# Kernel optimization log

Hardware: AMD Instinct MI355X
Metric: run time of the kernel (lower is better)

Reference implementation:

```python
import jax, jax.numpy as jnp
import numpy as np

N = 100000
E = 1600000
D_IN = 128
D_HID = 128
D_OUT = 64


def mish(x):
    return x * jnp.tanh(jax.nn.softplus(x))


def sage_conv(x, src, dst, W_l, b_l, W_r):
    # gather source-node features along edges, mean-aggregate at destination
    msg = x[src]  # [E, d]
    agg = jax.ops.segment_sum(msg, dst, num_segments=N)  # [N, d]
    cnt = jax.ops.segment_sum(jnp.ones((E,), x.dtype), dst, num_segments=N)
    agg = agg / jnp.maximum(cnt, 1.0)[:, None]
    # PyG SAGEConv: lin_l(aggregated) + lin_r(root); lin_r has no bias
    return agg @ W_l.T + b_l + x @ W_r.T


def setup_inputs() -> dict:
    key = jax.random.key(0)
    ks = jax.random.split(key, 10)
    s = lambda d: 1.0 / np.sqrt(d)
    return {
        "x": jax.random.normal(ks[0], (N, D_IN), jnp.float32),
        "edge_index": jax.random.randint(ks[1], (2, E), 0, N, jnp.int64),
        "W_l0": jax.random.normal(ks[2], (D_HID, D_IN), jnp.float32) * s(D_IN),
        "b_l0": jnp.zeros((D_HID,), jnp.float32),
        "W_r0": jax.random.normal(ks[3], (D_HID, D_IN), jnp.float32) * s(D_IN),
        "W_l1": jax.random.normal(ks[4], (D_HID, D_HID), jnp.float32) * s(D_HID),
        "b_l1": jnp.zeros((D_HID,), jnp.float32),
        "W_r1": jax.random.normal(ks[5], (D_HID, D_HID), jnp.float32) * s(D_HID),
        "W_head": jax.random.normal(ks[6], (D_OUT, D_HID), jnp.float32) * s(D_HID),
        "b_head": jnp.zeros((D_OUT,), jnp.float32),
    }


def reference(x, edge_index, W_l0, b_l0, W_r0, W_l1, b_l1, W_r1, W_head, b_head):
    src, dst = edge_index[0], edge_index[1]
    h = mish(sage_conv(x, src, dst, W_l0, b_l0, W_r0))  # dropout is identity in eval
    h = mish(sage_conv(h, src, dst, W_l1, b_l1, W_r1))
    return h @ W_head.T + b_head
```

## Files before the change

### kernel.cpp

```cpp
#include <hip/hip_runtime.h>
#include <math.h>

#define N_NODES 100000
#define N_EDGES 1600000
#define DF      128
#define D_HEAD  64

#define NWIN    256
#define WIN_SZ  391
#define NSEG    8
#define CAP_SEG 1024
#define BCH     8192
#define NBUCK   ((N_EDGES + BCH - 1) / BCH)

typedef __attribute__((ext_vector_type(8))) short bf16x8;
typedef __attribute__((ext_vector_type(4))) float f32x4;

static __device__ __forceinline__ float mish_f(float v) {
    float e = __expf(v);
    float q = 1.0f + e;
    float p = q * q;
    float m = v * (p - 1.0f) / (p + 1.0f);
    return (v > 40.0f) ? v : m;
}

static __device__ __forceinline__ unsigned short f2bf(float f) {
    unsigned int u = __builtin_bit_cast(unsigned int, f);
    unsigned int r = (u + 0x7fffu + ((u >> 16) & 1u)) >> 16;
    return (unsigned short)r;
}


__global__ void zero_cnt_kernel(int* __restrict__ bucket_cnt) {
    bucket_cnt[blockIdx.x * 256 + threadIdx.x] = 0;
}


#define XB 12500
#define WB 288

__global__ __launch_bounds__(256) void cvt_bucket_kernel(
        const float* __restrict__ x,
        const float* __restrict__ Wl0, const float* __restrict__ Wr0,
        const float* __restrict__ Wl1, const float* __restrict__ Wr1,
        const float* __restrict__ Wh,
        const int* __restrict__ src, const int* __restrict__ dst,
        unsigned short* __restrict__ xb, unsigned short* __restrict__ wb,
        int* __restrict__ bucket_cnt, unsigned int* __restrict__ pairs) {
    __shared__ int cnt[NWIN][4];
    __shared__ int cur[NWIN][4];
    int b   = blockIdx.x;
    int tid = threadIdx.x;

    if (b >= NBUCK) {
        int cb = b - NBUCK;
        if (cb < XB) {
            int i = cb * 256 + tid;
            float4 v = ((const float4*)x)[i];
            ushort4 o;
            o.x = f2bf(v.x); o.y = f2bf(v.y); o.z = f2bf(v.z); o.w = f2bf(v.w);
            ((ushort4*)xb)[i] = o;
        } else {
            int id = (cb - XB) * 256 + tid;
            if (id < 65536) {
                int seg = id >> 14;
                int r   = id & 16383;
                const float* W = (seg == 0) ? Wl0 : (seg == 1) ? Wr0 : (seg == 2) ? Wl1 : Wr1;
                wb[id] = f2bf(W[r]);
            } else {
                wb[id] = f2bf(Wh[id - 65536]);
            }
        }
        return;
    }

    int set = tid & 3;
    int sg  = b & 7;
    int e0  = b * BCH;
    for (int i = tid; i < NWIN * 4; i += 256) ((int*)cnt)[i] = 0;
    __syncthreads();

    int dc[BCH / 256];
    #pragma unroll 4
    for (int i = 0; i < BCH / 256; ++i) {
        int e = e0 + tid + i * 256;
        int d = (e < N_EDGES) ? dst[e] : -1;
        dc[i] = d;
        if (d >= 0) atomicAdd(&cnt[d / WIN_SZ][set], 1);
    }
    __syncthreads();
    for (int w = tid; w < NWIN; w += 256) {
        int c0 = cnt[w][0], c1 = cnt[w][1], c2 = cnt[w][2], c3 = cnt[w][3];
        int base = atomicAdd(&bucket_cnt[sg * NWIN + w], c0 + c1 + c2 + c3);
        cur[w][0] = base;
        cur[w][1] = base + c0;
        cur[w][2] = base + c0 + c1;
        cur[w][3] = base + c0 + c1 + c2;
    }
    __syncthreads();
    #pragma unroll 4
    for (int i = 0; i < BCH / 256; ++i) {
        int d = dc[i];
        if (d >= 0) {
            int e  = e0 + tid + i * 256;
            int s  = src[e];
            int w  = d / WIN_SZ;
            int dl = d - w * WIN_SZ;
            int idx = atomicAdd(&cur[w][set], 1);
            if (idx < CAP_SEG)
                pairs[((size_t)sg * NWIN + w) * CAP_SEG + idx] = (unsigned)s | ((unsigned)dl << 17);
        }
    }
}


__global__ __launch_bounds__(256) void build_win(const unsigned int* __restrict__ pairs,
                                                 const int* __restrict__ bucket_cnt,
                                                 int* __restrict__ rowstart,
                                                 int* __restrict__ csr) {
    __shared__ int ldeg[WIN_SZ];
    __shared__ int lcsr[NSEG * CAP_SEG];
    __shared__ int tot[NWIN];
    __shared__ int wsum[4];
    __shared__ int red[4];

    int tid = threadIdx.x;
    int w   = blockIdx.x;
    int base_node = w * WIN_SZ;
    int nn = N_NODES - base_node;
    if (nn > WIN_SZ) nn = WIN_SZ;
    if (nn < 0) nn = 0;

    {
        int t = 0;
        #pragma unroll
        for (int s2 = 0; s2 < NSEG; ++s2) {
            int c = bucket_cnt[s2 * NWIN + tid];
            t += (c > CAP_SEG) ? CAP_SEG : c;
        }
        tot[tid] = t;
    }
    for (int i = tid; i < WIN_SZ; i += 256) ldeg[i] = 0;
    __syncthreads();

    int val = (tid < w) ? tot[tid] : 0;
    #pragma unroll
    for (int o = 32; o; o >>= 1) val += __shfl_xor(val, o);
    if ((tid & 63) == 0) red[tid >> 6] = val;
    int ntot = tot[w];
    __syncthreads();
    int ebase = red[0] + red[1] + red[2] + red[3];

    #pragma unroll
    for (int s2 = 0; s2 < NSEG; ++s2) {
        int c = bucket_cnt[s2 * NWIN + w];
        if (c > CAP_SEG) c = CAP_SEG;
        const unsigned int* pw = pairs + ((size_t)s2 * NWIN + w) * CAP_SEG;
        for (int i = tid; i < c; i += 256)
            atomicAdd(&ldeg[pw[i] >> 17], 1);
    }
    __syncthreads();

    int i0 = tid * 2;
    int v[2];
    int s = 0;
    #pragma unroll
    for (int q = 0; q < 2; ++q) {
        v[q] = (i0 + q < nn) ? ldeg[i0 + q] : 0;
        s += v[q];
    }
    int lane = tid & 63, wv = tid >> 6;
    int sc = s;
    #pragma unroll
    for (int d = 1; d < 64; d <<= 1) {
        int t = __shfl_up(sc, d);
        if (lane >= d) sc += t;
    }
    if (lane == 63) wsum[wv] = sc;
    __syncthreads();
    int woff = 0;
    for (int q = 0; q < wv; ++q) woff += wsum[q];
    int run = woff + sc - s;
    #pragma unroll
    for (int q = 0; q < 2; ++q) {
        if (i0 + q < nn) {
            rowstart[base_node + i0 + q] = ebase + run;
            ldeg[i0 + q] = run;
            run += v[q];
        }
    }
    if (w == NWIN - 1 && tid == 0) rowstart[N_NODES] = N_EDGES;
    __syncthreads();

    #pragma unroll
    for (int s2 = 0; s2 < NSEG; ++s2) {
        int c = bucket_cnt[s2 * NWIN + w];
        if (c > CAP_SEG) c = CAP_SEG;
        const unsigned int* pw = pairs + ((size_t)s2 * NWIN + w) * CAP_SEG;
        for (int i = tid; i < c; i += 256) {
            unsigned int p = pw[i];
            int slot = atomicAdd(&ldeg[p >> 17], 1);
            lcsr[slot] = (int)(p & 0x1FFFFu);
        }
    }
    __syncthreads();

    for (int i = tid; i < ntot; i += 256)
        csr[ebase + i] = lcsr[i];
}


__global__ __launch_bounds__(256) void aggregate_kernel(const unsigned short* __restrict__ X,
                                                        const int* __restrict__ rowstart,
                                                        const int* __restrict__ csr,
                                                        unsigned short* __restrict__ out) {
    int wv   = threadIdx.x >> 6;
    int lane = threadIdx.x & 63;
    int slot = lane >> 4;
    int l16  = lane & 15;
    int wid  = blockIdx.x * 4 + wv;
    int n0 = wid;
    int n1 = wid + (N_NODES / 2);

    int a0 = rowstart[n0], a1 = rowstart[n0 + 1];
    int b0 = rowstart[n1], b1 = rowstart[n1 + 1];

    int ca[4], cb[4];
    #pragma unroll
    for (int j = 0; j < 4; ++j) {
        int ea = a0 + 4 * j + slot;
        int eb = b0 + 4 * j + slot;
        ca[j] = (ea < a1) ? csr[ea] : -1;
        cb[j] = (eb < b1) ? csr[eb] : -1;
    }
    uint4 va[4], vb[4];
    #pragma unroll
    for (int j = 0; j < 4; ++j) {
        uint4 t = {0u, 0u, 0u, 0u};
        if (ca[j] >= 0) t = *(const uint4*)(X + (size_t)ca[j] * DF + l16 * 8);
        va[j] = t;
    }
    #pragma unroll
    for (int j = 0; j < 4; ++j) {
        uint4 t = {0u, 0u, 0u, 0u};
        if (cb[j] >= 0) t = *(const uint4*)(X + (size_t)cb[j] * DF + l16 * 8);
        vb[j] = t;
    }

    float accA[8], accB[8];
    #pragma unroll
    for (int i = 0; i < 8; ++i) { accA[i] = 0.f; accB[i] = 0.f; }

    #pragma unroll
    for (int j = 0; j < 4; ++j) {
        unsigned int w0[4] = {va[j].x, va[j].y, va[j].z, va[j].w};
        #pragma unroll
        for (int i = 0; i < 4; ++i) {
            accA[2 * i]     += __builtin_bit_cast(float, w0[i] << 16);
            accA[2 * i + 1] += __builtin_bit_cast(float, w0[i] & 0xffff0000u);
        }
    }
    #pragma unroll
    for (int j = 0; j < 4; ++j) {
        unsigned int w0[4] = {vb[j].x, vb[j].y, vb[j].z, vb[j].w};
        #pragma unroll
        for (int i = 0; i < 4; ++i) {
            accB[2 * i]     += __builtin_bit_cast(float, w0[i] << 16);
            accB[2 * i + 1] += __builtin_bit_cast(float, w0[i] & 0xffff0000u);
        }
    }

    for (int e0 = a0 + 16; e0 < a1; e0 += 16) {
        uint4 v[4];
        #pragma unroll
        for (int j = 0; j < 4; ++j) {
            int e = e0 + 4 * j + slot;
            uint4 t = {0u, 0u, 0u, 0u};
            if (e < a1) t = *(const uint4*)(X + (size_t)csr[e] * DF + l16 * 8);
            v[j] = t;
        }
        #pragma unroll
        for (int j = 0; j < 4; ++j) {
            unsigned int w0[4] = {v[j].x, v[j].y, v[j].z, v[j].w};
            #pragma unroll
            for (int i = 0; i < 4; ++i) {
                accA[2 * i]     += __builtin_bit_cast(float, w0[i] << 16);
                accA[2 * i + 1] += __builtin_bit_cast(float, w0[i] & 0xffff0000u);
            }
        }
    }
    for (int e0 = b0 + 16; e0 < b1; e0 += 16) {
        uint4 v[4];
        #pragma unroll
        for (int j = 0; j < 4; ++j) {
            int e = e0 + 4 * j + slot;
            uint4 t = {0u, 0u, 0u, 0u};
            if (e < b1) t = *(const uint4*)(X + (size_t)csr[e] * DF + l16 * 8);
            v[j] = t;
        }
        #pragma unroll
        for (int j = 0; j < 4; ++j) {
            unsigned int w0[4] = {v[j].x, v[j].y, v[j].z, v[j].w};
            #pragma unroll
            for (int i = 0; i < 4; ++i) {
                accB[2 * i]     += __builtin_bit_cast(float, w0[i] << 16);
                accB[2 * i + 1] += __builtin_bit_cast(float, w0[i] & 0xffff0000u);
            }
        }
    }

    #pragma unroll
    for (int i = 0; i < 8; ++i) {
        accA[i] += __shfl_xor(accA[i], 32);
        accA[i] += __shfl_xor(accA[i], 16);
        accB[i] += __shfl_xor(accB[i], 32);
        accB[i] += __shfl_xor(accB[i], 16);
    }

    int dA = a1 - a0, dB = b1 - b0;
    float invA = 1.0f / (float)(dA > 0 ? dA : 1);
    float invB = 1.0f / (float)(dB > 0 ? dB : 1);
    if (slot == 0) {
        unsigned int r[4];
        #pragma unroll
        for (int i = 0; i < 4; ++i) {
            unsigned int lo = f2bf(accA[2 * i] * invA);
            unsigned int hi = f2bf(accA[2 * i + 1] * invA);
            r[i] = lo | (hi << 16);
        }
        uint4 o = {r[0], r[1], r[2], r[3]};
        *(uint4*)(out + (size_t)n0 * DF + l16 * 8) = o;
    } else if (slot == 1) {
        unsigned int r[4];
        #pragma unroll
        for (int i = 0; i < 4; ++i) {
            unsigned int lo = f2bf(accB[2 * i] * invB);
            unsigned int hi = f2bf(accB[2 * i + 1] * invB);
            r[i] = lo | (hi << 16);
        }
        uint4 o = {r[0], r[1], r[2], r[3]};
        *(uint4*)(out + (size_t)n1 * DF + l16 * 8) = o;
    }
}


template <int COLS, bool TWO, bool MISH, bool OUT_BF16>
__global__ __launch_bounds__(256, 3) void sage_gemm(const unsigned short* __restrict__ A,
                                                    const unsigned short* __restrict__ H,
                                                    const unsigned short* __restrict__ Wl,
                                                    const unsigned short* __restrict__ Wr,
                                                    const float* __restrict__ bias,
                                                    void* __restrict__ out) {
    constexpr int NT  = COLS / 16;
    constexpr int LDA = 136;
    __shared__ unsigned short Ws[COLS * LDA];

    int tid  = threadIdx.x;
    int wv   = tid >> 6;
    int lane = tid & 63;
    int quad = lane >> 4;
    int l16  = lane & 15;
    int m0   = blockIdx.x * 128;

    int arow0 = m0 + wv * 32 + l16;
    int arow1 = arow0 + 16;
    if (arow0 > N_NODES - 1) arow0 = N_NODES - 1;
    if (arow1 > N_NODES - 1) arow1 = N_NODES - 1;

    f32x4 acc[2][NT];
    #pragma unroll
    for (int t = 0; t < 2; ++t)
        #pragma unroll
        for (int n = 0; n < NT; ++n) acc[t][n] = (f32x4){0.f, 0.f, 0.f, 0.f};

    #pragma unroll
    for (int phase = 0; phase < (TWO ? 2 : 1); ++phase) {
        const unsigned short* Ain = phase ? H : A;
        const unsigned short* Win = phase ? Wr : Wl;
        if (phase) __syncthreads();
        #pragma unroll
        for (int i = 0; i < COLS / 16; ++i) {
            int idx = tid + i * 256;
            int r   = idx >> 4;
            int cb  = (idx & 15) * 8;
            *(uint4*)&Ws[r * LDA + cb] = *(const uint4*)&Win[r * 128 + cb];
        }
        __syncthreads();

        const unsigned short* Ap0 = Ain + (size_t)arow0 * 128 + quad * 8;
        const unsigned short* Ap1 = Ain + (size_t)arow1 * 128 + quad * 8;
        #pragma unroll
        for (int ks = 0; ks < 4; ++ks) {
            bf16x8 af0 = *(const bf16x8*)(Ap0 + ks * 32);
            bf16x8 af1 = *(const bf16x8*)(Ap1 + ks * 32);
            #pragma unroll
            for (int n = 0; n < NT; ++n) {
                bf16x8 bfr = *(const bf16x8*)&Ws[(n * 16 + l16) * LDA + ks * 32 + quad * 8];
                acc[0][n] = __builtin_amdgcn_mfma_f32_16x16x32_bf16(af0, bfr, acc[0][n], 0, 0, 0);
                acc[1][n] = __builtin_amdgcn_mfma_f32_16x16x32_bf16(af1, bfr, acc[1][n], 0, 0, 0);
            }
        }
    }

    #pragma unroll
    for (int t = 0; t < 2; ++t) {
        #pragma unroll
        for (int n = 0; n < NT; ++n) {
            int col = n * 16 + l16;
            float b = bias[col];
            #pragma unroll
            for (int r = 0; r < 4; ++r) {
                int row = m0 + wv * 32 + t * 16 + quad * 4 + r;
                if (row < N_NODES) {
                    float v = acc[t][n][r] + b;
                    if constexpr (MISH) v = mish_f(v);
                    if constexpr (OUT_BF16)
                        ((unsigned short*)out)[(size_t)row * COLS + col] = f2bf(v);
                    else
                        ((float*)out)[(size_t)row * COLS + col] = v;
                }
            }
        }
    }
}


__global__ __launch_bounds__(256, 3) void sage_gemm1_head(const unsigned short* __restrict__ A,
                                                          const unsigned short* __restrict__ H,
                                                          const unsigned short* __restrict__ Wl,
                                                          const unsigned short* __restrict__ Wr,
                                                          const float* __restrict__ bias,
                                                          const unsigned short* __restrict__ Wh,
                                                          const float* __restrict__ bh,
                                                          float* __restrict__ out) {
    constexpr int LDA = 136;
    __shared__ unsigned short Ws[128 * LDA];

    int tid  = threadIdx.x;
    int wv   = tid >> 6;
    int lane = tid & 63;
    int quad = lane >> 4;
    int l16  = lane & 15;
    int m0   = blockIdx.x * 128;

    int arow0 = m0 + wv * 32 + l16;
    int arow1 = arow0 + 16;
    if (arow0 > N_NODES - 1) arow0 = N_NODES - 1;
    if (arow1 > N_NODES - 1) arow1 = N_NODES - 1;

    f32x4 acc0[2][8];
    #pragma unroll
    for (int t = 0; t < 2; ++t)
        #pragma unroll
        for (int n = 0; n < 8; ++n) acc0[t][n] = (f32x4){0.f, 0.f, 0.f, 0.f};

    #pragma unroll
    for (int phase = 0; phase < 2; ++phase) {
        const unsigned short* Ain = phase ? H : A;
        const unsigned short* Win = phase ? Wr : Wl;
        if (phase) __syncthreads();
        #pragma unroll
        for (int i = 0; i < 8; ++i) {
            int idx = tid + i * 256;
            int r   = idx >> 4;
            int cb  = (idx & 15) * 8;
            *(uint4*)&Ws[r * LDA + cb] = *(const uint4*)&Win[r * 128 + cb];
        }
        __syncthreads();

        const unsigned short* Ap0 = Ain + (size_t)arow0 * 128 + quad * 8;
        const unsigned short* Ap1 = Ain + (size_t)arow1 * 128 + quad * 8;
        #pragma unroll
        for (int ks = 0; ks < 4; ++ks) {
            bf16x8 af0 = *(const bf16x8*)(Ap0 + ks * 32);
            bf16x8 af1 = *(const bf16x8*)(Ap1 + ks * 32);
            #pragma unroll
            for (int n = 0; n < 8; ++n) {
                bf16x8 bfr = *(const bf16x8*)&Ws[(n * 16 + l16) * LDA + ks * 32 + quad * 8];
                acc0[0][n] = __builtin_amdgcn_mfma_f32_16x16x32_bf16(af0, bfr, acc0[0][n], 0, 0, 0);
                acc0[1][n] = __builtin_amdgcn_mfma_f32_16x16x32_bf16(af1, bfr, acc0[1][n], 0, 0, 0);
            }
        }
    }
    __syncthreads();

    #pragma unroll
    for (int t = 0; t < 2; ++t) {
        #pragma unroll
        for (int n = 0; n < 8; ++n) {
            int col = n * 16 + l16;
            float b = bias[col];
            #pragma unroll
            for (int r = 0; r < 4; ++r) {
                int row = wv * 32 + t * 16 + quad * 4 + r;
                Ws[row * LDA + col] = f2bf(mish_f(acc0[t][n][r] + b));
            }
        }
    }
    __syncthreads();

    f32x4 acc2[2][4];
    #pragma unroll
    for (int t = 0; t < 2; ++t)
        #pragma unroll
        for (int n = 0; n < 4; ++n) acc2[t][n] = (f32x4){0.f, 0.f, 0.f, 0.f};

    int ar0 = wv * 32 + l16;
    #pragma unroll
    for (int ks = 0; ks < 4; ++ks) {
        bf16x8 af0 = *(const bf16x8*)&Ws[ar0 * LDA + ks * 32 + quad * 8];
        bf16x8 af1 = *(const bf16x8*)&Ws[(ar0 + 16) * LDA + ks * 32 + quad * 8];
        #pragma unroll
        for (int n = 0; n < 4; ++n) {
            bf16x8 bfr = *(const bf16x8*)&Wh[(n * 16 + l16) * 128 + ks * 32 + quad * 8];
            acc2[0][n] = __builtin_amdgcn_mfma_f32_16x16x32_bf16(af0, bfr, acc2[0][n], 0, 0, 0);
            acc2[1][n] = __builtin_amdgcn_mfma_f32_16x16x32_bf16(af1, bfr, acc2[1][n], 0, 0, 0);
        }
    }

    #pragma unroll
    for (int t = 0; t < 2; ++t) {
        #pragma unroll
        for (int n = 0; n < 4; ++n) {
            int col = n * 16 + l16;
            float b = bh[col];
            #pragma unroll
            for (int r = 0; r < 4; ++r) {
                int row = m0 + wv * 32 + t * 16 + quad * 4 + r;
                if (row < N_NODES)
                    out[(size_t)row * D_HEAD + col] = acc2[t][n][r] + b;
            }
        }
    }
}


extern "C" void kernel_launch(void* const* d_in, const int* in_sizes, int n_in,
                              void* d_out, int out_size, void* d_ws, size_t ws_size,
                              hipStream_t stream) {
    const float* x   = (const float*)d_in[0];
    const int*   ei  = (const int*)d_in[1];
    const float* Wl0 = (const float*)d_in[2];
    const float* bl0 = (const float*)d_in[3];
    const float* Wr0 = (const float*)d_in[4];
    const float* Wl1 = (const float*)d_in[5];
    const float* bl1 = (const float*)d_in[6];
    const float* Wr1 = (const float*)d_in[7];
    const float* Wh  = (const float*)d_in[8];
    const float* bh  = (const float*)d_in[9];
    float* out = (float*)d_out;

    const int* src = ei;
    const int* dst = ei + N_EDGES;

    char* ws = (char*)d_ws;
    size_t off = 0;
    auto alloc = [&](size_t bytes) -> void* {
        void* p = ws + off;
        off += (bytes + 255) & ~(size_t)255;
        return p;
    };
    int* rowstart   = (int*)alloc((N_NODES + 1) * 4);
    int* csr        = (int*)alloc(N_EDGES * 4);
    int* bucket_cnt = (int*)alloc(NSEG * NWIN * 4);

    unsigned short* Wb  = (unsigned short*)alloc((size_t)(65536 + 8192) * 2);
    unsigned short* Xb  = (unsigned short*)alloc((size_t)N_NODES * DF * 2);
    unsigned short* Ab  = (unsigned short*)alloc((size_t)N_NODES * DF * 2);
    unsigned short* H1b = (unsigned short*)alloc((size_t)N_NODES * DF * 2);

    unsigned short* Wlb0 = Wb;
    unsigned short* Wrb0 = Wb + 16384;
    unsigned short* Wlb1 = Wb + 32768;
    unsigned short* Wrb1 = Wb + 49152;
    unsigned short* Whb  = Wb + 65536;
    unsigned int* pairs  = (unsigned int*)H1b;

    zero_cnt_kernel<<<NSEG, 256, 0, stream>>>(bucket_cnt);

    cvt_bucket_kernel<<<NBUCK + XB + WB, 256, 0, stream>>>(
        x, Wl0, Wr0, Wl1, Wr1, Wh, src, dst, Xb, Wb, bucket_cnt, pairs);

    build_win<<<NWIN, 256, 0, stream>>>(pairs, bucket_cnt, rowstart, csr);

    aggregate_kernel<<<N_NODES / 8, 256, 0, stream>>>(Xb, rowstart, csr, Ab);
    const int grid = (N_NODES + 127) / 128;
    sage_gemm<128, true, true, true><<<grid, 256, 0, stream>>>(Ab, Xb, Wlb0, Wrb0, bl0, H1b);
    aggregate_kernel<<<N_NODES / 8, 256, 0, stream>>>(H1b, rowstart, csr, Ab);
    sage_gemm1_head<<<grid, 256, 0, stream>>>(Ab, H1b, Wlb1, Wrb1, bl1, Whb, bh, out);
}
```

Before: 331.4 us.

## Fuse zeroing, bucketing, conversion and CSR build into one cooperative kernel

Merges the counter-zero kernel, the edge bucketing/bf16 conversion kernel and the window CSR build kernel into a single cooperative launch of 256 blocks separated by grid-wide syncs. This removes two kernel launches and their inter-kernel gaps. In exchange only 256 blocks run the edge bucketing and x conversion, so each block handles more edges and grid-strides over the conversion, which lowers parallelism and leaves most of the GPU idle. The fused kernel also uses more shared memory per block, which could limit co-residency.

```diff
diff --git a/kernel.cpp b/kernel.cpp
--- a/kernel.cpp
+++ b/kernel.cpp
@@ -1,5 +1,8 @@
 #include <hip/hip_runtime.h>
+#include <hip/hip_cooperative_groups.h>
 #include <math.h>
+
+namespace cg = cooperative_groups;
 
 #define N_NODES 100000
 #define N_EDGES 1600000
@@ -10,8 +13,8 @@
 #define WIN_SZ  391
 #define NSEG    8
 #define CAP_SEG 1024
-#define BCH     8192
-#define NBUCK   ((N_EDGES + BCH - 1) / BCH)
+#define EPB     (N_EDGES / NWIN)
+#define EITER   ((EPB + 255) / 256)
 
 typedef __attribute__((ext_vector_type(8))) short bf16x8;
 typedef __attribute__((ext_vector_type(4))) float f32x4;
@@ -31,65 +34,47 @@
 }
 
 
-__global__ void zero_cnt_kernel(int* __restrict__ bucket_cnt) {
-    bucket_cnt[blockIdx.x * 256 + threadIdx.x] = 0;
-}
-
-
-#define XB 12500
-#define WB 288
-
-__global__ __launch_bounds__(256) void cvt_bucket_kernel(
+__global__ __launch_bounds__(256) void prep_kernel(
         const float* __restrict__ x,
         const float* __restrict__ Wl0, const float* __restrict__ Wr0,
         const float* __restrict__ Wl1, const float* __restrict__ Wr1,
         const float* __restrict__ Wh,
         const int* __restrict__ src, const int* __restrict__ dst,
         unsigned short* __restrict__ xb, unsigned short* __restrict__ wb,
-        int* __restrict__ bucket_cnt, unsigned int* __restrict__ pairs) {
+        int* __restrict__ bucket_cnt, unsigned int* __restrict__ pairs,
+        int* __restrict__ rowstart, int* __restrict__ csr) {
     __shared__ int cnt[NWIN][4];
     __shared__ int cur[NWIN][4];
+    __shared__ int ldeg[WIN_SZ];
+    __shared__ int lcsr[NSEG * CAP_SEG];
+    __shared__ int tot[NWIN];
+    __shared__ int wsum[4];
+    __shared__ int red[4];
+
+    cg::grid_group grid = cg::this_grid();
     int b   = blockIdx.x;
     int tid = threadIdx.x;
 
-    if (b >= NBUCK) {
-        int cb = b - NBUCK;
-        if (cb < XB) {
-            int i = cb * 256 + tid;
-            float4 v = ((const float4*)x)[i];
-            ushort4 o;
-            o.x = f2bf(v.x); o.y = f2bf(v.y); o.z = f2bf(v.z); o.w = f2bf(v.w);
-            ((ushort4*)xb)[i] = o;
-        } else {
-            int id = (cb - XB) * 256 + tid;
-            if (id < 65536) {
-                int seg = id >> 14;
-                int r   = id & 16383;
-                const float* W = (seg == 0) ? Wl0 : (seg == 1) ? Wr0 : (seg == 2) ? Wl1 : Wr1;
-                wb[id] = f2bf(W[r]);
-            } else {
-                wb[id] = f2bf(Wh[id - 65536]);
-            }
-        }
-        return;
-    }
+    if (b < NSEG) bucket_cnt[b * NWIN + tid] = 0;
+    grid.sync();
 
     int set = tid & 3;
     int sg  = b & 7;
-    int e0  = b * BCH;
+    int e0  = b * EPB;
     for (int i = tid; i < NWIN * 4; i += 256) ((int*)cnt)[i] = 0;
     __syncthreads();
 
-    int dc[BCH / 256];
-    #pragma unroll 4
-    for (int i = 0; i < BCH / 256; ++i) {
+    int dc[EITER];
+    #pragma unroll
+    for (int i = 0; i < EITER; ++i) {
         int e = e0 + tid + i * 256;
-        int d = (e < N_EDGES) ? dst[e] : -1;
+        int d = (e < e0 + EPB) ? dst[e] : -1;
         dc[i] = d;
         if (d >= 0) atomicAdd(&cnt[d / WIN_SZ][set], 1);
     }
     __syncthreads();
-    for (int w = tid; w < NWIN; w += 256) {
+    {
+        int w = tid;
         int c0 = cnt[w][0], c1 = cnt[w][1], c2 = cnt[w][2], c3 = cnt[w][3];
         int base = atomicAdd(&bucket_cnt[sg * NWIN + w], c0 + c1 + c2 + c3);
         cur[w][0] = base;
@@ -98,8 +83,8 @@
         cur[w][3] = base + c0 + c1 + c2;
     }
     __syncthreads();
-    #pragma unroll 4
-    for (int i = 0; i < BCH / 256; ++i) {
+    #pragma unroll
+    for (int i = 0; i < EITER; ++i) {
         int d = dc[i];
         if (d >= 0) {
             int e  = e0 + tid + i * 256;
@@ -111,21 +96,32 @@
                 pairs[((size_t)sg * NWIN + w) * CAP_SEG + idx] = (unsigned)s | ((unsigned)dl << 17);
         }
     }
-}
-
-
-__global__ __launch_bounds__(256) void build_win(const unsigned int* __restrict__ pairs,
-                                                 const int* __restrict__ bucket_cnt,
-                                                 int* __restrict__ rowstart,
-                                                 int* __restrict__ csr) {
-    __shared__ int ldeg[WIN_SZ];
-    __shared__ int lcsr[NSEG * CAP_SEG];
-    __shared__ int tot[NWIN];
-    __shared__ int wsum[4];
-    __shared__ int red[4];
-
-    int tid = threadIdx.x;
-    int w   = blockIdx.x;
+
+    {
+        const int TT = NWIN * 256;
+        int gtid = b * 256 + tid;
+        for (int i = gtid; i < N_NODES * DF / 4; i += TT) {
+            float4 v = ((const float4*)x)[i];
+            ushort4 o;
+            o.x = f2bf(v.x); o.y = f2bf(v.y); o.z = f2bf(v.z); o.w = f2bf(v.w);
+            ((ushort4*)xb)[i] = o;
+        }
+        for (int id = gtid; id < 65536 + 8192; id += TT) {
+            if (id < 65536) {
+                int seg = id >> 14;
+                int r   = id & 16383;
+                const float* W = (seg == 0) ? Wl0 : (seg == 1) ? Wr0 : (seg == 2) ? Wl1 : Wr1;
+                wb[id] = f2bf(W[r]);
+            } else {
+                wb[id] = f2bf(Wh[id - 65536]);
+            }
+        }
+    }
+
+    __threadfence();
+    grid.sync();
+
+    int w = b;
     int base_node = w * WIN_SZ;
     int nn = N_NODES - base_node;
     if (nn > WIN_SZ) nn = WIN_SZ;
@@ -576,12 +572,15 @@
     unsigned short* Whb  = Wb + 65536;
     unsigned int* pairs  = (unsigned int*)H1b;
 
-    zero_cnt_kernel<<<NSEG, 256, 0, stream>>>(bucket_cnt);
-
-    cvt_bucket_kernel<<<NBUCK + XB + WB, 256, 0, stream>>>(
-        x, Wl0, Wr0, Wl1, Wr1, Wh, src, dst, Xb, Wb, bucket_cnt, pairs);
-
-    build_win<<<NWIN, 256, 0, stream>>>(pairs, bucket_cnt, rowstart, csr);
+    unsigned short* xb = Xb;
+    unsigned short* wb = Wb;
+    void* args[] = {
+        (void*)&x, (void*)&Wl0, (void*)&Wr0, (void*)&Wl1, (void*)&Wr1, (void*)&Wh,
+        (void*)&src, (void*)&dst, (void*)&xb, (void*)&wb,
+        (void*)&bucket_cnt, (void*)&pairs, (void*)&rowstart, (void*)&csr
+    };
+    hipLaunchCooperativeKernel((const void*)prep_kernel, dim3(NWIN), dim3(256),
+                               args, 0, stream);
 
     aggregate_kernel<<<N_NODES / 8, 256, 0, stream>>>(Xb, rowstart, csr, Ab);
     const int grid = (N_NODES + 127) / 128;
```

Result: slower. 432.2 us (+30.4%).
